# Kernel tuning notes

Measured on AMD Instinct MI355X. Metric: run time of the kernel, lower is better.

Reference implementation:

```python
import jax, jax.numpy as jnp
import numpy as np
from jax import lax

NUM_CLUSTER = 128
N_ITERS = 10


def setup_inputs() -> dict:
    key = jax.random.key(0)
    feat_g = jax.random.normal(key, (131072, 256), dtype=jnp.float32)
    return {"feat_g": feat_g}


def _sq_dists(x, c):
    x2 = jnp.sum(x * x, axis=1, keepdims=True)            # [N,1]
    c2 = jnp.sum(c * c, axis=1)                           # [K]
    return x2 - 2.0 * (x @ c.T) + c2[None, :]


def _kmeans_fit(x, k, iters):
    n = x.shape[0]
    init_c = x[:k]  # deterministic init: first k points
    ones = jnp.ones((n,), dtype=x.dtype)

    def step(c, _):
        assign = jnp.argmin(_sq_dists(x, c), axis=1)                 # [N]
        sums = jax.ops.segment_sum(x, assign, num_segments=k)       # [K,d]
        counts = jax.ops.segment_sum(ones, assign, num_segments=k)  # [K]
        new_c = sums / jnp.maximum(counts, 1.0)[:, None]
        new_c = jnp.where(counts[:, None] > 0, new_c, c)  # keep empty clusters
        return new_c, None

    c, _ = lax.scan(step, init_c, None, length=iters)
    return c


def reference(feat_g):
    # view(batch, -1, dim) then view(-1, dim) is an identity reshape for the math
    x = lax.stop_gradient(feat_g)  # original detaches feat_gc before fit/predict
    c = _kmeans_fit(x, NUM_CLUSTER, N_ITERS)
    preds = jnp.argmin(_sq_dists(x, c), axis=1)  # [N] int labels
    return preds
```

## Files before the change

### kernel.cpp

```cpp
#include <hip/hip_runtime.h>

#define NPTS 131072
#define DIM 256
#define NK 128
#define NITER 10
#define SEG 16
#define TILE 128
#define MAXSEGS (NPTS / TILE + NK)

typedef _Float16 half8 __attribute__((ext_vector_type(8)));
typedef _Float16 half4v __attribute__((ext_vector_type(4)));
typedef float f32x4 __attribute__((ext_vector_type(4)));

#define RSCALE 4096.0f
#define RINV 2.44140625e-4f

__global__ void x2_kernel(const float* __restrict__ x, float* __restrict__ x2) {
  int tid = threadIdx.x;
  int p = blockIdx.x * 16 + (tid >> 4);
  int part = tid & 15;
  const float4* xr = (const float4*)(x + (size_t)p * DIM);
  float s = 0.f;
#pragma unroll
  for (int j = 0; j < 4; ++j) {
    float4 v = xr[part * 4 + j];
    s += v.x * v.x;
    s += v.y * v.y;
    s += v.z * v.z;
    s += v.w * v.w;
  }
#pragma unroll
  for (int m = 8; m >= 1; m >>= 1) s += __shfl_xor(s, m, 16);
  if (part == 0) x2[p] = s;
}

__global__ void c2_kernel(const float* __restrict__ c, float* __restrict__ c2) {
  int k = blockIdx.x, lane = threadIdx.x;
  float4 v = ((const float4*)(c + (size_t)k * DIM))[lane];
  float s = v.x * v.x + v.y * v.y + v.z * v.z + v.w * v.w;
#pragma unroll
  for (int m = 32; m >= 1; m >>= 1) s += __shfl_xor(s, m, 64);
  if (lane == 0) c2[k] = s;
}

__global__ void convert_x_kernel(const float* __restrict__ x, _Float16* __restrict__ x1,
                                 _Float16* __restrict__ x2s) {
  int i = blockIdx.x * 256 + threadIdx.x;
  float4 v = ((const float4*)x)[i];
  float f[4] = {v.x, v.y, v.z, v.w};
  half4v h, l;
#pragma unroll
  for (int j = 0; j < 4; ++j) {
    _Float16 hi = (_Float16)f[j];
    float r = f[j] - (float)hi;
    h[j] = hi;
    l[j] = (_Float16)(r * RSCALE);
  }
  ((half4v*)x1)[i] = h;
  ((half4v*)x2s)[i] = l;
}

__global__ void convert_c_kernel(const float* __restrict__ c, _Float16* __restrict__ ct) {
  int i = blockIdx.x * 256 + threadIdx.x;
  int k = i >> 6;
  int d4 = i & 63;
  float4 v = ((const float4*)c)[i];
  float f[4] = {v.x, v.y, v.z, v.w};
  half4v h, l;
#pragma unroll
  for (int j = 0; j < 4; ++j) {
    _Float16 hi = (_Float16)f[j];
    float r = f[j] - (float)hi;
    h[j] = hi;
    l[j] = (_Float16)(r * RSCALE);
  }
  int ch = d4 >> 3;
  int idx4 = ch * 2048 + k * 8 + (d4 & 7);
  ((half4v*)ct)[idx4] = h;
  ((half4v*)ct)[idx4 + 1024] = l;
}

template <bool DOHIST>
__global__ __launch_bounds__(256, 2) void assign_mfma_kernel(
    const _Float16* __restrict__ x1, const _Float16* __restrict__ x2s,
    const _Float16* __restrict__ ct, const float* __restrict__ x2,
    const float* __restrict__ c2, int* __restrict__ out, int* __restrict__ hist) {
  __shared__ __align__(16) _Float16 cbuf[2][8192];
  __shared__ int hcnt[NK];

  int tid = threadIdx.x;
  int lane = tid & 63;
  int w = tid >> 6;
  int lcol = lane & 15;
  int lgrp = lane >> 4;
  int row0 = blockIdx.x * 128 + w * 32;

  if (DOHIST && tid < NK) hcnt[tid] = 0;

  const _Float16* xa = x1 + (size_t)(row0 + lcol) * DIM + lgrp * 8;
  const _Float16* xb = x2s + (size_t)(row0 + lcol) * DIM + lgrp * 8;
  const half8* ctv = (const half8*)ct;

  f32x4 acc1[2][8], acc2[2][8];
#pragma unroll
  for (int rt = 0; rt < 2; ++rt)
#pragma unroll
    for (int c8 = 0; c8 < 8; ++c8) {
      acc1[rt][c8] = f32x4{0.f, 0.f, 0.f, 0.f};
      acc2[rt][c8] = f32x4{0.f, 0.f, 0.f, 0.f};
    }

  half8 A1[2], A2[2], nA1[2], nA2[2], sreg[4];

#pragma unroll
  for (int r = 0; r < 4; ++r) sreg[r] = ctv[r * 256 + tid];
#pragma unroll
  for (int rt = 0; rt < 2; ++rt) {
    A1[rt] = *(const half8*)(xa + rt * 16 * DIM);
    A2[rt] = *(const half8*)(xb + rt * 16 * DIM);
  }
#pragma unroll
  for (int r = 0; r < 4; ++r) ((half8*)cbuf[0])[r * 256 + tid] = sreg[r];
  __syncthreads();

#pragma unroll
  for (int ck = 0; ck < 8; ++ck) {
    const int cb = ck & 1;
    if (ck < 7) {
#pragma unroll
      for (int r = 0; r < 4; ++r) sreg[r] = ctv[(ck + 1) * 1024 + r * 256 + tid];
#pragma unroll
      for (int rt = 0; rt < 2; ++rt) {
        nA1[rt] = *(const half8*)(xa + rt * 16 * DIM + (ck + 1) * 32);
        nA2[rt] = *(const half8*)(xb + rt * 16 * DIM + (ck + 1) * 32);
      }
    }
#pragma unroll
    for (int c8 = 0; c8 < 8; ++c8) {
      int bidx = (c8 * 16 + lcol) * 32 + lgrp * 8;
      half8 b1 = *(const half8*)&cbuf[cb][bidx];
      half8 b2 = *(const half8*)&cbuf[cb][4096 + bidx];
#pragma unroll
      for (int rt = 0; rt < 2; ++rt) {
        acc1[rt][c8] = __builtin_amdgcn_mfma_f32_16x16x32_f16(A1[rt], b1, acc1[rt][c8], 0, 0, 0);
        acc2[rt][c8] = __builtin_amdgcn_mfma_f32_16x16x32_f16(A1[rt], b2, acc2[rt][c8], 0, 0, 0);
        acc2[rt][c8] = __builtin_amdgcn_mfma_f32_16x16x32_f16(A2[rt], b1, acc2[rt][c8], 0, 0, 0);
      }
    }
    if (ck < 7) {
#pragma unroll
      for (int r = 0; r < 4; ++r) ((half8*)cbuf[cb ^ 1])[r * 256 + tid] = sreg[r];
#pragma unroll
      for (int rt = 0; rt < 2; ++rt) {
        A1[rt] = nA1[rt];
        A2[rt] = nA2[rt];
      }
      __syncthreads();
    }
  }

#pragma unroll
  for (int rt = 0; rt < 2; ++rt) {
    int pbase = row0 + rt * 16 + lgrp * 4;
    float x2p[4];
#pragma unroll
    for (int r = 0; r < 4; ++r) x2p[r] = x2[pbase + r];
    float bv[4];
    int bk[4];
#pragma unroll
    for (int r = 0; r < 4; ++r) { bv[r] = 3.4e38f; bk[r] = 0; }
#pragma unroll
    for (int c8 = 0; c8 < 8; ++c8) {
      int kc = c8 * 16 + lcol;
      float c2k = c2[kc];
#pragma unroll
      for (int r = 0; r < 4; ++r) {
        float dot = fmaf(acc2[rt][c8][r], RINV, acc1[rt][c8][r]);
        float d = fmaf(-2.f, dot, x2p[r]) + c2k;
        if (d < bv[r]) { bv[r] = d; bk[r] = kc; }
      }
    }
#pragma unroll
    for (int m = 1; m <= 8; m <<= 1) {
#pragma unroll
      for (int r = 0; r < 4; ++r) {
        float ov = __shfl_xor(bv[r], m, 64);
        int ok = __shfl_xor(bk[r], m, 64);
        if (ov < bv[r] || (ov == bv[r] && ok < bk[r])) { bv[r] = ov; bk[r] = ok; }
      }
    }
    if (lcol == 0) {
#pragma unroll
      for (int r = 0; r < 4; ++r) {
        out[pbase + r] = bk[r];
        if (DOHIST) atomicAdd(&hcnt[bk[r]], 1);
      }
    }
  }

  if (DOHIST) {
    __syncthreads();
    if (tid < NK) {
      int v = hcnt[tid];
      if (v) atomicAdd(&hist[(blockIdx.x >> 3) * NK + tid], v);
    }
  }
}

__global__ void assign_kernel(const float* __restrict__ x, const float* __restrict__ c,
                              const float* __restrict__ x2, const float* __restrict__ c2,
                              int* __restrict__ assign_out) {
  __shared__ float4 xs4[64 * 4];
  __shared__ float4 cs4[128 * 4];
  __shared__ float redv[64][17];
  __shared__ int redk[64][17];

  int tid = threadIdx.x;
  int tx = tid & 15;
  int ty = tid >> 4;
  int row0 = blockIdx.x * 64;

  float acc[4][8];
#pragma unroll
  for (int a = 0; a < 4; ++a)
#pragma unroll
    for (int b = 0; b < 8; ++b) acc[a][b] = 0.f;

  for (int ck = 0; ck < 16; ++ck) {
    {
      int p = tid >> 2, d4 = tid & 3;
      float4 v = *(const float4*)(x + (size_t)(row0 + p) * DIM + ck * 16 + d4 * 4);
      xs4[p * 4 + (d4 ^ ((p >> 2) & 3))] = v;
    }
#pragma unroll
    for (int r = 0; r < 2; ++r) {
      int idx = tid + r * 256;
      int kk = idx >> 2, dd = idx & 3;
      float4 v = *(const float4*)(c + (size_t)kk * DIM + ck * 16 + dd * 4);
      cs4[kk * 4 + (dd ^ ((kk >> 3) & 3))] = v;
    }
    __syncthreads();
#pragma unroll
    for (int d4 = 0; d4 < 4; ++d4) {
      float4 xr[4], cr[8];
#pragma unroll
      for (int pp = 0; pp < 4; ++pp) xr[pp] = xs4[(tx * 4 + pp) * 4 + (d4 ^ (tx & 3))];
#pragma unroll
      for (int kk = 0; kk < 8; ++kk) cr[kk] = cs4[(ty * 8 + kk) * 4 + (d4 ^ (ty & 3))];
#pragma unroll
      for (int pp = 0; pp < 4; ++pp)
#pragma unroll
        for (int kk = 0; kk < 8; ++kk) {
          acc[pp][kk] = fmaf(xr[pp].x, cr[kk].x, acc[pp][kk]);
          acc[pp][kk] = fmaf(xr[pp].y, cr[kk].y, acc[pp][kk]);
          acc[pp][kk] = fmaf(xr[pp].z, cr[kk].z, acc[pp][kk]);
          acc[pp][kk] = fmaf(xr[pp].w, cr[kk].w, acc[pp][kk]);
        }
    }
    __syncthreads();
  }

  float x2p[4];
#pragma unroll
  for (int pp = 0; pp < 4; ++pp) x2p[pp] = x2[row0 + tx * 4 + pp];

  float bestv[4];
  int bestk[4];
#pragma unroll
  for (int pp = 0; pp < 4; ++pp) { bestv[pp] = 3.4e38f; bestk[pp] = 0; }
#pragma unroll
  for (int kk = 0; kk < 8; ++kk) {
    float c2k = c2[ty * 8 + kk];
#pragma unroll
    for (int pp = 0; pp < 4; ++pp) {
      float d = fmaf(-2.f, acc[pp][kk], x2p[pp]) + c2k;
      if (d < bestv[pp]) { bestv[pp] = d; bestk[pp] = ty * 8 + kk; }
    }
  }
#pragma unroll
  for (int pp = 0; pp < 4; ++pp) {
    redv[tx * 4 + pp][ty] = bestv[pp];
    redk[tx * 4 + pp][ty] = bestk[pp];
  }
  __syncthreads();
  if (tid < 64) {
    float bv = redv[tid][0];
    int bk = redk[tid][0];
#pragma unroll
    for (int t = 1; t < 16; ++t) {
      float v = redv[tid][t];
      if (v < bv) { bv = v; bk = redk[tid][t]; }
    }
    assign_out[row0 + tid] = bk;
  }
}

__global__ void hist_kernel(const int* __restrict__ assign_in, int* __restrict__ hist) {
  __shared__ int h[NK];
  int tid = threadIdx.x, b = blockIdx.x;
  if (tid < NK) h[tid] = 0;
  __syncthreads();
#pragma unroll
  for (int r = 0; r < 4; ++r) {
    int a = assign_in[b * 1024 + r * 256 + tid];
    atomicAdd(&h[a], 1);
  }
  __syncthreads();
  if (tid < NK) hist[b * NK + tid] = h[tid];
}

__global__ void scan_kernel(int* __restrict__ hist, int* __restrict__ base,
                            int* __restrict__ counts, int* __restrict__ cbase,
                            int* __restrict__ segbase) {
  __shared__ int h[128 * NK];
  __shared__ int scnt[NK];
  __shared__ int scb[NK];
  __shared__ int ssb[NK + 1];
  int tid = threadIdx.x;
  for (int i = tid; i < 128 * NK; i += 256) h[i] = hist[i];
  __syncthreads();
  for (int i = tid; i < 128 * NK; i += 256) hist[i] = 0;
  if (tid < NK) {
    int run = 0;
    for (int b = 0; b < 128; ++b) {
      int v = h[b * NK + tid];
      h[b * NK + tid] = run;
      run += v;
    }
    scnt[tid] = run;
    counts[tid] = run;
  }
  __syncthreads();
  if (tid == 0) {
    int cb = 0, sb = 0;
    for (int j = 0; j < NK; ++j) {
      scb[j] = cb;
      cb += scnt[j];
      ssb[j] = sb;
      sb += (scnt[j] + TILE - 1) / TILE;
    }
    ssb[NK] = sb;
  }
  __syncthreads();
  if (tid < NK) {
    cbase[tid] = scb[tid];
    int cbk = scb[tid];
    for (int b = 0; b < 128; ++b) base[b * NK + tid] = h[b * NK + tid] + cbk;
  }
  if (tid <= NK) segbase[tid] = ssb[tid];
}

__global__ void scatter_kernel(const int* __restrict__ assign_in, const int* __restrict__ base,
                               int* __restrict__ perm) {
  __shared__ int cnt[NK];
  int lane = threadIdx.x, b = blockIdx.x;
  cnt[lane] = base[b * NK + lane];
  cnt[lane + 64] = base[b * NK + lane + 64];
  for (int r = 0; r < 16; ++r) {
    int p = b * 1024 + r * 64 + lane;
    int a = assign_in[p];
    unsigned long long mask = ~0ull;
#pragma unroll
    for (int j = 0; j < 7; ++j) {
      unsigned long long bal = __ballot((a >> j) & 1);
      mask &= ((a >> j) & 1) ? bal : ~bal;
    }
    int rank = __popcll(mask & ((1ull << lane) - 1ull));
    int pos = cnt[a] + rank;
    perm[pos] = p;
    if (rank == 0) cnt[a] += (int)__popcll(mask);
  }
}

__global__ __launch_bounds__(256) void seg_sum_v3_kernel(
    const float* __restrict__ x, const int* __restrict__ perm,
    const int* __restrict__ counts, const int* __restrict__ cbase,
    const int* __restrict__ segbase, float* __restrict__ partial) {
  __shared__ int sb[NK + 1];
  __shared__ float4 red[4][64];
  int tid = threadIdx.x;
  if (tid <= NK) sb[tid] = segbase[tid];
  __syncthreads();
  int b = blockIdx.x;
  if (b >= sb[NK]) return;
  int lo = 0, hi = NK - 1;
  while (lo < hi) {
    int mid = (lo + hi + 1) >> 1;
    if (sb[mid] <= b) lo = mid;
    else hi = mid - 1;
  }
  int k = lo;
  int cnt = counts[k], off = cbase[k];
  int j0 = (b - sb[k]) * TILE;
  int j1 = min(j0 + TILE, cnt);

  int tg = tid >> 6;
  int lane = tid & 63;
  int len = j1 - j0;
  int jj0 = j0 + (len * tg) / 4;
  int jj1 = j0 + (len * (tg + 1)) / 4;
  int n = jj1 - jj0;

  int pv = 0;
  if (lane < n) pv = perm[off + jj0 + lane];

  float4 acc = {0.f, 0.f, 0.f, 0.f};
#pragma unroll 4
  for (int j = 0; j < n; ++j) {
    int p = __shfl(pv, j, 64);
    float4 v = ((const float4*)(x + (size_t)p * DIM))[lane];
    acc.x += v.x;
    acc.y += v.y;
    acc.z += v.z;
    acc.w += v.w;
  }
  red[tg][lane] = acc;
  __syncthreads();
  if (tg == 0) {
    float4 s0 = red[0][lane], s1 = red[1][lane], s2 = red[2][lane], s3 = red[3][lane];
    float4 t;
    t.x = ((s0.x + s1.x) + s2.x) + s3.x;
    t.y = ((s0.y + s1.y) + s2.y) + s3.y;
    t.z = ((s0.z + s1.z) + s2.z) + s3.z;
    t.w = ((s0.w + s1.w) + s2.w) + s3.w;
    ((float4*)(partial + (size_t)b * DIM))[lane] = t;
  }
}

__global__ void reduce_kernel(const float* __restrict__ partial, const int* __restrict__ counts,
                              const int* __restrict__ segbase, float* __restrict__ c,
                              float* __restrict__ c2, _Float16* __restrict__ ct) {
  __shared__ float wsum[4];
  int k = blockIdx.x, d = threadIdx.x;
  int cnt = counts[k];
  int s0 = segbase[k], s1 = segbase[k + 1];
  float s = 0.f;
  int t = s0;
  for (; t + 4 <= s1; t += 4) {
    float p0 = partial[(size_t)(t + 0) * DIM + d];
    float p1 = partial[(size_t)(t + 1) * DIM + d];
    float p2 = partial[(size_t)(t + 2) * DIM + d];
    float p3 = partial[(size_t)(t + 3) * DIM + d];
    s += ((p0 + p1) + p2) + p3;
  }
  for (; t < s1; ++t) s += partial[(size_t)t * DIM + d];

  float nc;
  if (cnt > 0)
    nc = s / fmaxf((float)cnt, 1.0f);
  else
    nc = c[(size_t)k * DIM + d];
  c[(size_t)k * DIM + d] = nc;

  {
    _Float16 hi = (_Float16)nc;
    float r = nc - (float)hi;
    _Float16 lov = (_Float16)(r * RSCALE);
    int ch = d >> 5, dd = d & 31;
    ct[ch * 8192 + k * 32 + dd] = hi;
    ct[ch * 8192 + k * 32 + dd + 4096] = lov;
  }

  float s2 = nc * nc;
#pragma unroll
  for (int m = 32; m >= 1; m >>= 1) s2 += __shfl_xor(s2, m, 64);
  if ((threadIdx.x & 63) == 0) wsum[threadIdx.x >> 6] = s2;
  __syncthreads();
  if (threadIdx.x == 0) c2[k] = wsum[0] + wsum[1] + wsum[2] + wsum[3];
}

__global__ void seg_sum_kernel(const float* __restrict__ x, const int* __restrict__ perm,
                               const int* __restrict__ counts, const int* __restrict__ cbase,
                               float* __restrict__ partial) {
  int k = blockIdx.x, s = blockIdx.y, d = threadIdx.x;
  int cnt = counts[k], off = cbase[k];
  int j0 = (int)(((long long)cnt * s) / SEG);
  int j1 = (int)(((long long)cnt * (s + 1)) / SEG);
  float sum = 0.f;
  int j = j0;
  for (; j + 4 <= j1; j += 4) {
    int p0 = perm[off + j + 0];
    int p1 = perm[off + j + 1];
    int p2 = perm[off + j + 2];
    int p3 = perm[off + j + 3];
    sum += x[(size_t)p0 * DIM + d];
    sum += x[(size_t)p1 * DIM + d];
    sum += x[(size_t)p2 * DIM + d];
    sum += x[(size_t)p3 * DIM + d];
  }
  for (; j < j1; ++j) sum += x[(size_t)perm[off + j] * DIM + d];
  partial[((size_t)k * SEG + s) * DIM + d] = sum;
}

__global__ void reduce_fb_kernel(const float* __restrict__ partial, const int* __restrict__ counts,
                                 float* __restrict__ c, float* __restrict__ c2) {
  __shared__ float wsum[4];
  int k = blockIdx.x, d = threadIdx.x;
  int cnt = counts[k];
  float s = 0.f;
#pragma unroll
  for (int t = 0; t < SEG; ++t) s += partial[((size_t)k * SEG + t) * DIM + d];
  float nc;
  if (cnt > 0)
    nc = s / fmaxf((float)cnt, 1.0f);
  else
    nc = c[(size_t)k * DIM + d];
  c[(size_t)k * DIM + d] = nc;
  float s2 = nc * nc;
#pragma unroll
  for (int m = 32; m >= 1; m >>= 1) s2 += __shfl_xor(s2, m, 64);
  if ((threadIdx.x & 63) == 0) wsum[threadIdx.x >> 6] = s2;
  __syncthreads();
  if (threadIdx.x == 0) c2[k] = wsum[0] + wsum[1] + wsum[2] + wsum[3];
}

__global__ void scan_fb_kernel(const int* __restrict__ hist, int* __restrict__ base,
                               int* __restrict__ counts, int* __restrict__ cbase) {
  __shared__ int h[128 * NK];
  int tid = threadIdx.x;
  for (int i = tid; i < 128 * NK; i += 256) h[i] = hist[i];
  __syncthreads();
  if (tid < NK) {
    int run = 0;
    for (int b = 0; b < 128; ++b) {
      int v = h[b * NK + tid];
      h[b * NK + tid] = run;
      run += v;
    }
    counts[tid] = run;
  }
  __syncthreads();
  if (tid == 0) {
    int cb = 0;
    for (int j = 0; j < NK; ++j) {
      cbase[j] = cb;
      cb += counts[j];
    }
  }
  __syncthreads();
  if (tid < NK) {
    int cbk = cbase[tid];
    for (int b = 0; b < 128; ++b) base[b * NK + tid] = h[b * NK + tid] + cbk;
  }
}

extern "C" void kernel_launch(void* const* d_in, const int* in_sizes, int n_in,
                              void* d_out, int out_size, void* d_ws, size_t ws_size,
                              hipStream_t stream) {
  const float* x = (const float*)d_in[0];
  char* ws = (char*)d_ws;

  const size_t NEED_BIG = 138283520;
  bool use_mfma = ws_size >= NEED_BIG;

  if (use_mfma) {
    _Float16* x1 = (_Float16*)(ws + 0);
    _Float16* x2s = (_Float16*)(ws + 67108864);
    float* c = (float*)(ws + 134217728);
    _Float16* ct = (_Float16*)(ws + 134348800);
    float* c2 = (float*)(ws + 134479872);
    float* x2 = (float*)(ws + 134480384);
    int* assignb = (int*)(ws + 135004672);
    int* hist = (int*)(ws + 135528960);
    int* base = (int*)(ws + 135594496);
    int* counts = (int*)(ws + 135660032);
    int* cbase = (int*)(ws + 135660544);
    int* perm = (int*)(ws + 135661056);
    float* partial = (float*)(ws + 136185344);
    int* segbase = (int*)(ws + 138282496);

    hipMemcpyAsync(c, x, (size_t)NK * DIM * sizeof(float), hipMemcpyDeviceToDevice, stream);
    hipMemsetAsync(hist, 0, 128 * NK * sizeof(int), stream);
    convert_x_kernel<<<NPTS * DIM / 4 / 256, 256, 0, stream>>>(x, x1, x2s);
    x2_kernel<<<NPTS / 16, 256, 0, stream>>>(x, x2);
    c2_kernel<<<NK, 64, 0, stream>>>(c, c2);
    convert_c_kernel<<<NK * DIM / 4 / 256, 256, 0, stream>>>(c, ct);

    for (int it = 0; it < NITER; ++it) {
      assign_mfma_kernel<true><<<NPTS / 128, 256, 0, stream>>>(x1, x2s, ct, x2, c2, assignb, hist);
      scan_kernel<<<1, 256, 0, stream>>>(hist, base, counts, cbase, segbase);
      scatter_kernel<<<NPTS / 1024, 64, 0, stream>>>(assignb, base, perm);
      seg_sum_v3_kernel<<<MAXSEGS, 256, 0, stream>>>(x, perm, counts, cbase, segbase, partial);
      reduce_kernel<<<NK, 256, 0, stream>>>(partial, counts, segbase, c, c2, ct);
    }
    assign_mfma_kernel<false><<<NPTS / 128, 256, 0, stream>>>(x1, x2s, ct, x2, c2, (int*)d_out,
                                                              hist);
  } else {
    float* c = (float*)(ws + 0);
    float* c2 = (float*)(ws + 131072);
    float* x2 = (float*)(ws + 132096);
    int* assignb = (int*)(ws + 656384);
    int* hist = (int*)(ws + 1180672);
    int* base = (int*)(ws + 1246208);
    int* counts = (int*)(ws + 1311744);
    int* cbase = (int*)(ws + 1312256);
    int* perm = (int*)(ws + 1312768);
    float* partial = (float*)(ws + 1837056);

    hipMemcpyAsync(c, x, (size_t)NK * DIM * sizeof(float), hipMemcpyDeviceToDevice, stream);
    x2_kernel<<<NPTS / 16, 256, 0, stream>>>(x, x2);
    c2_kernel<<<NK, 64, 0, stream>>>(c, c2);

    for (int it = 0; it < NITER; ++it) {
      assign_kernel<<<NPTS / 64, 256, 0, stream>>>(x, c, x2, c2, assignb);
      hist_kernel<<<NPTS / 1024, 256, 0, stream>>>(assignb, hist);
      scan_fb_kernel<<<1, 256, 0, stream>>>(hist, base, counts, cbase);
      scatter_kernel<<<NPTS / 1024, 64, 0, stream>>>(assignb, base, perm);
      seg_sum_kernel<<<dim3(NK, SEG), 256, 0, stream>>>(x, perm, counts, cbase, partial);
      reduce_fb_kernel<<<NK, 256, 0, stream>>>(partial, counts, c, c2);
    }
    assign_kernel<<<NPTS / 64, 256, 0, stream>>>(x, c, x2, c2, (int*)d_out);
  }
}
```

Baseline: 1.029 ms.

## Fuse x conversion with norm computation and read split-half data in segment sums

Merges the fp16 hi/lo split conversion and the squared-norm computation into a single kernel, so x is read once instead of twice during setup. The segment-sum kernel now gathers rows from the two fp16 arrays (hi and scaled residual) rather than the fp32 input. Each point then costs two 512-byte gathers instead of one 1 KB gather, which halves nothing in bytes but may fit better in cache alongside the assign kernel's working set. The reconstructed values are slightly less exact than the original fp32, so centroid sums can drift a little.

```diff
diff --git a/kernel.cpp b/kernel.cpp
--- a/kernel.cpp
+++ b/kernel.cpp
@@ -43,21 +43,34 @@
   if (lane == 0) c2[k] = s;
 }
 
-__global__ void convert_x_kernel(const float* __restrict__ x, _Float16* __restrict__ x1,
-                                 _Float16* __restrict__ x2s) {
-  int i = blockIdx.x * 256 + threadIdx.x;
-  float4 v = ((const float4*)x)[i];
-  float f[4] = {v.x, v.y, v.z, v.w};
-  half4v h, l;
+__global__ void convert_x2_kernel(const float* __restrict__ x, _Float16* __restrict__ x1,
+                                  _Float16* __restrict__ x2s, float* __restrict__ x2) {
+  int tid = threadIdx.x;
+  int p = blockIdx.x * 16 + (tid >> 4);
+  int part = tid & 15;
+  const float4* xr = (const float4*)(x + (size_t)p * DIM);
+  half4v* o1 = (half4v*)(x1 + (size_t)p * DIM);
+  half4v* o2 = (half4v*)(x2s + (size_t)p * DIM);
+  float s = 0.f;
 #pragma unroll
   for (int j = 0; j < 4; ++j) {
-    _Float16 hi = (_Float16)f[j];
-    float r = f[j] - (float)hi;
-    h[j] = hi;
-    l[j] = (_Float16)(r * RSCALE);
-  }
-  ((half4v*)x1)[i] = h;
-  ((half4v*)x2s)[i] = l;
+    float4 v = xr[part * 4 + j];
+    float f[4] = {v.x, v.y, v.z, v.w};
+    half4v h, l;
+#pragma unroll
+    for (int u = 0; u < 4; ++u) {
+      _Float16 hi = (_Float16)f[u];
+      float r = f[u] - (float)hi;
+      h[u] = hi;
+      l[u] = (_Float16)(r * RSCALE);
+      s += f[u] * f[u];
+    }
+    o1[part * 4 + j] = h;
+    o2[part * 4 + j] = l;
+  }
+#pragma unroll
+  for (int m = 8; m >= 1; m >>= 1) s += __shfl_xor(s, m, 16);
+  if (part == 0) x2[p] = s;
 }
 
 __global__ void convert_c_kernel(const float* __restrict__ c, _Float16* __restrict__ ct) {
@@ -372,10 +385,11 @@
   }
 }
 
-__global__ __launch_bounds__(256) void seg_sum_v3_kernel(
-    const float* __restrict__ x, const int* __restrict__ perm,
-    const int* __restrict__ counts, const int* __restrict__ cbase,
-    const int* __restrict__ segbase, float* __restrict__ partial) {
+__global__ __launch_bounds__(256) void seg_sum_v4_kernel(
+    const _Float16* __restrict__ x1, const _Float16* __restrict__ x2s,
+    const int* __restrict__ perm, const int* __restrict__ counts,
+    const int* __restrict__ cbase, const int* __restrict__ segbase,
+    float* __restrict__ partial) {
   __shared__ int sb[NK + 1];
   __shared__ float4 red[4][64];
   int tid = threadIdx.x;
@@ -408,11 +422,12 @@
 #pragma unroll 4
   for (int j = 0; j < n; ++j) {
     int p = __shfl(pv, j, 64);
-    float4 v = ((const float4*)(x + (size_t)p * DIM))[lane];
-    acc.x += v.x;
-    acc.y += v.y;
-    acc.z += v.z;
-    acc.w += v.w;
+    half4v h = ((const half4v*)(x1 + (size_t)p * DIM))[lane];
+    half4v l = ((const half4v*)(x2s + (size_t)p * DIM))[lane];
+    acc.x += fmaf((float)l[0], RINV, (float)h[0]);
+    acc.y += fmaf((float)l[1], RINV, (float)h[1]);
+    acc.z += fmaf((float)l[2], RINV, (float)h[2]);
+    acc.w += fmaf((float)l[3], RINV, (float)h[3]);
   }
   red[tg][lane] = acc;
   __syncthreads();
@@ -571,8 +586,7 @@
 
     hipMemcpyAsync(c, x, (size_t)NK * DIM * sizeof(float), hipMemcpyDeviceToDevice, stream);
     hipMemsetAsync(hist, 0, 128 * NK * sizeof(int), stream);
-    convert_x_kernel<<<NPTS * DIM / 4 / 256, 256, 0, stream>>>(x, x1, x2s);
-    x2_kernel<<<NPTS / 16, 256, 0, stream>>>(x, x2);
+    convert_x2_kernel<<<NPTS / 16, 256, 0, stream>>>(x, x1, x2s, x2);
     c2_kernel<<<NK, 64, 0, stream>>>(c, c2);
     convert_c_kernel<<<NK * DIM / 4 / 256, 256, 0, stream>>>(c, ct);
 
@@ -580,7 +594,8 @@
       assign_mfma_kernel<true><<<NPTS / 128, 256, 0, stream>>>(x1, x2s, ct, x2, c2, assignb, hist);
       scan_kernel<<<1, 256, 0, stream>>>(hist, base, counts, cbase, segbase);
       scatter_kernel<<<NPTS / 1024, 64, 0, stream>>>(assignb, base, perm);
-      seg_sum_v3_kernel<<<MAXSEGS, 256, 0, stream>>>(x, perm, counts, cbase, segbase, partial);
+      seg_sum_v4_kernel<<<MAXSEGS, 256, 0, stream>>>(x1, x2s, perm, counts, cbase, segbase,
+                                                     partial);
       reduce_kernel<<<NK, 256, 0, stream>>>(partial, counts, segbase, c, c2, ct);
     }
     assign_mfma_kernel<false><<<NPTS / 128, 256, 0, stream>>>(x1, x2s, ct, x2, c2, (int*)d_out,
```

Result: faster. 993.5 us (-3.4%).
